# Performance work log

Hardware: AMD Instinct MI355X
Metric: run time of the kernel (lower is better)

Reference implementation:

```python
import jax, jax.numpy as jnp
import numpy as np

B, S, HID = 2, 2048, 2048
NH, NKV, HD = 16, 4, 128  # num_heads, num_kv_heads, head_dim; kqv_size = NH*HD = 2048
KV_DIM = NKV * HD  # 512


def setup_inputs() -> dict:
    key = jax.random.key(0)
    ks = jax.random.split(key, 7)
    sc = 0.02
    return {
        "hidden_states": jax.random.normal(ks[0], (B, S, HID), dtype=jnp.float32),
        "Wq": jax.random.normal(ks[1], (NH * HD, HID), dtype=jnp.float32) * sc,
        "Wk": jax.random.normal(ks[2], (KV_DIM, HID), dtype=jnp.float32) * sc,
        "Wv": jax.random.normal(ks[3], (KV_DIM, HID), dtype=jnp.float32) * sc,
        "Wo": jax.random.normal(ks[4], (HID, NH * HD), dtype=jnp.float32) * sc,
        "bo": jnp.zeros((HID,), dtype=jnp.float32),
    }


def reference(hidden_states, Wq, Wk, Wv, Wo, bo):
    b, s, _ = hidden_states.shape
    # projections (nn.Linear: x @ W.T), no bias on q/k/v
    q = (hidden_states @ Wq.T).reshape(b, s, NH, HD).transpose(0, 2, 1, 3)   # [B,NH,S,HD]
    k = (hidden_states @ Wk.T).reshape(b, s, NKV, HD).transpose(0, 2, 1, 3)  # [B,NKV,S,HD]
    v = (hidden_states @ Wv.T).reshape(b, s, NKV, HD).transpose(0, 2, 1, 3)
    # GQA: query head h uses kv head h // (NH // NKV)
    g = NH // NKV
    k_rep = jnp.repeat(k, g, axis=1)  # [B,NH,S,HD]
    v_rep = jnp.repeat(v, g, axis=1)
    # float32 upcast, NO 1/sqrt(d) scaling (GPT-Neo style)
    qf = q.astype(jnp.float32)
    kf = k_rep.astype(jnp.float32)
    scores = jnp.einsum("bhqd,bhkd->bhqk", qf, kf)  # [B,NH,S,S]
    causal = jnp.tril(jnp.ones((s, s), dtype=bool))[None, None]
    neg = jnp.finfo(scores.dtype).min
    scores = jnp.where(causal, scores, neg)
    attn = jax.nn.softmax(scores, axis=-1).astype(v.dtype)  # dropout p=0 (eval)
    out = jnp.einsum("bhqk,bhkd->bhqd", attn, v_rep)         # [B,NH,S,HD]
    out = out.transpose(0, 2, 1, 3).reshape(b, s, NH * HD)
    return out @ Wo.T + bo
```

## Files before the change

### kernel.cpp

```cpp
#include <hip/hip_runtime.h>

typedef _Float16 f16;
typedef __attribute__((ext_vector_type(4))) _Float16 f16x4;
typedef __attribute__((ext_vector_type(8))) _Float16 f16x8;
typedef __attribute__((ext_vector_type(4))) float f32x4;

#define NB 2
#define NS 2048
#define NHID 2048
#define N_H 16
#define N_KV 4
#define N_HD 128

__device__ __forceinline__ void gload16(void* lds, const void* g) {
  __builtin_amdgcn_global_load_lds(
      (const __attribute__((address_space(1))) unsigned int*)g,
      (__attribute__((address_space(3))) unsigned int*)lds, 16, 0, 0);
}

__global__ __launch_bounds__(256) void cvt_kernel(const float* __restrict__ in,
                                                  f16* __restrict__ out, int n4) {
  int i = blockIdx.x * 256 + threadIdx.x;
  if (i >= n4) return;
  const float4 v = reinterpret_cast<const float4*>(in)[i];
  f16x4 o = {(f16)v.x, (f16)v.y, (f16)v.z, (f16)v.w};
  reinterpret_cast<f16x4*>(out)[i] = o;
}

__global__ __launch_bounds__(256) void cvt3_kernel(const float* __restrict__ a, int na4,
                                                   const float* __restrict__ b, int nb4,
                                                   const float* __restrict__ c, int nc4,
                                                   f16* __restrict__ out) {
  int i = blockIdx.x * 256 + threadIdx.x;
  if (i >= na4 + nb4 + nc4) return;
  const float* src;
  int j;
  if (i < na4) { src = a; j = i; }
  else if (i < na4 + nb4) { src = b; j = i - na4; }
  else { src = c; j = i - na4 - nb4; }
  const float4 v = reinterpret_cast<const float4*>(src)[j];
  f16x4 o = {(f16)v.x, (f16)v.y, (f16)v.z, (f16)v.w};
  reinterpret_cast<f16x4*>(out)[i] = o;
}

template <int MODE>
__global__ __launch_bounds__(256) void gemm_bt(
    const f16* __restrict__ A, const f16* __restrict__ Bm, int K,
    f16* __restrict__ q_out, f16* __restrict__ k_out, f16* __restrict__ v_out,
    float* __restrict__ f_out, const float* __restrict__ bias) {
  __shared__ f16 Alds[128 * 32];
  __shared__ f16 Blds[128 * 32];
  const int t = threadIdx.x;
  const int l = t & 63;
  const int w = t >> 6;
  const int g = l >> 4;
  const int l15 = l & 15;
  const int mb = blockIdx.y, nb = blockIdx.x;
  const int wr = w >> 1, wc = w & 1;

  f32x4 acc[4][4] = {};
  const int nK = K >> 5;
  for (int kb = 0; kb < nK; ++kb) {
    __syncthreads();
#pragma unroll
    for (int it = 0; it < 2; ++it) {
      int cb = w * 128 + it * 64;
      int c = cb + l;
      int row = c >> 2, ci = c & 3;
      gload16(Alds + cb * 8, A + (size_t)(mb * 128 + row) * K + kb * 32 + ci * 8);
      gload16(Blds + cb * 8, Bm + (size_t)(nb * 128 + row) * K + kb * 32 + ci * 8);
    }
    asm volatile("s_waitcnt vmcnt(0)" ::: "memory");
    __syncthreads();

    f16x8 af[4], bf[4];
#pragma unroll
    for (int mi = 0; mi < 4; ++mi)
      af[mi] = *reinterpret_cast<const f16x8*>(Alds + (wr * 64 + mi * 16 + l15) * 32 + g * 8);
#pragma unroll
    for (int ni = 0; ni < 4; ++ni)
      bf[ni] = *reinterpret_cast<const f16x8*>(Blds + (wc * 64 + ni * 16 + l15) * 32 + g * 8);
#pragma unroll
    for (int mi = 0; mi < 4; ++mi)
#pragma unroll
      for (int ni = 0; ni < 4; ++ni)
        acc[mi][ni] = __builtin_amdgcn_mfma_f32_16x16x32_f16(af[mi], bf[ni], acc[mi][ni], 0, 0, 0);
  }

#pragma unroll
  for (int mi = 0; mi < 4; ++mi) {
    int m0 = mb * 128 + wr * 64 + mi * 16 + 4 * g;
#pragma unroll
    for (int ni = 0; ni < 4; ++ni) {
      int n = nb * 128 + wc * 64 + ni * 16 + l15;
#pragma unroll
      for (int r = 0; r < 4; ++r) {
        int mm = m0 + r;
        float val = acc[mi][ni][r];
        if (MODE == 0) {
          int b = mm >> 11, s = mm & (NS - 1);
          if (n < 2048) {
            int h = n >> 7, d = n & 127;
            q_out[(((size_t)(b * N_H + h)) * NS + s) * N_HD + d] = (f16)val;
          } else if (n < 2560) {
            int n2 = n - 2048, kvh = n2 >> 7, d = n2 & 127;
            k_out[(((size_t)(b * N_KV + kvh)) * NS + s) * N_HD + d] = (f16)val;
          } else {
            int n3 = n - 2560, kvh = n3 >> 7, d = n3 & 127;
            v_out[(((size_t)(b * N_KV + kvh)) * NS + s) * N_HD + d] = (f16)val;
          }
        } else {
          f_out[(size_t)mm * NHID + n] = val + bias[n];
        }
      }
    }
  }
}

__global__ __launch_bounds__(256) void transpose_v(const f16* __restrict__ V,
                                                   f16* __restrict__ Vt) {
  __shared__ f16 tt[64][72];
  int s0 = blockIdx.x * 64, d0 = blockIdx.y * 64, bk = blockIdx.z;
  const f16* Vp = V + (size_t)bk * NS * N_HD;
  f16* Vtp = Vt + (size_t)bk * N_HD * NS;
  int tid = threadIdx.x;
#pragma unroll
  for (int it = 0; it < 2; ++it) {
    int c = it * 256 + tid;
    int sr = c >> 3, dc = (c & 7) * 8;
    f16x8 v = *reinterpret_cast<const f16x8*>(Vp + (size_t)(s0 + sr) * N_HD + d0 + dc);
#pragma unroll
    for (int j = 0; j < 8; ++j) tt[dc + j][sr] = v[j];
  }
  __syncthreads();
#pragma unroll
  for (int it = 0; it < 2; ++it) {
    int c = it * 256 + tid;
    int dr = c >> 3, sc = (c & 7) * 8;
    f16x8 o;
#pragma unroll
    for (int j = 0; j < 8; ++j) o[j] = tt[dr][sc + j];
    *reinterpret_cast<f16x8*>(Vtp + (size_t)(d0 + dr) * NS + s0 + sc) = o;
  }
}

__device__ __forceinline__ void stage_kv(const f16* __restrict__ Kp,
                                         const f16* __restrict__ Vp,
                                         f16* Kl, f16* Vl, int kt, int w, int l) {
#pragma unroll
  for (int it = 0; it < 4; ++it) {
    int cb = (it * 4 + w) * 64;
    int c = cb + l;
    int krow = c >> 4, pch = c & 15;
    int sch = (pch & 8) | ((pch ^ krow) & 7);
    gload16(Kl + cb * 8, Kp + (size_t)(kt * 64 + krow) * N_HD + sch * 8);
  }
#pragma unroll
  for (int it = 0; it < 4; ++it) {
    int cb = (it * 4 + w) * 64;
    int c = cb + l;
    int drow = c >> 3, pch = c & 7;
    int sch = (pch ^ drow) & 7;
    gload16(Vl + cb * 8, Vp + (size_t)drow * NS + kt * 64 + sch * 8);
  }
}

__device__ __forceinline__ void attn_step(
    const f16x8* qf, f32x4* oacc, float* mrow, float* lrow, int q0, int kt,
    const f16* Kl, const f16* Vl, f16* Pw, int g, int l15, bool diag) {
  f32x4 sacc[4];
#pragma unroll
  for (int nt = 0; nt < 4; ++nt) {
    f32x4 z = {0.f, 0.f, 0.f, 0.f};
#pragma unroll
    for (int ks = 0; ks < 4; ++ks) {
      int kr = nt * 16 + l15;
      int ch = ks * 4 + g;
      int sw = (ch & 8) | ((ch ^ kr) & 7);
      f16x8 kf = *reinterpret_cast<const f16x8*>(Kl + kr * 128 + sw * 8);
      z = __builtin_amdgcn_mfma_f32_16x16x32_f16(qf[ks], kf, z, 0, 0, 0);
    }
    sacc[nt] = z;
  }

  float p[4][4], alpha[4];
#pragma unroll
  for (int r = 0; r < 4; ++r) {
    int qg = q0 + r;
    float mx = -3.0e38f;
#pragma unroll
    for (int nt = 0; nt < 4; ++nt) {
      float sv = sacc[nt][r];
      if (diag) {
        int kg = kt * 64 + nt * 16 + l15;
        if (kg > qg) sv = -3.0e38f;
      }
      p[nt][r] = sv;
      mx = fmaxf(mx, sv);
    }
#pragma unroll
    for (int off = 8; off >= 1; off >>= 1) mx = fmaxf(mx, __shfl_xor(mx, off));
    float mn = fmaxf(mrow[r], mx);
    alpha[r] = __expf(mrow[r] - mn);
    mrow[r] = mn;
    float rs = 0.f;
#pragma unroll
    for (int nt = 0; nt < 4; ++nt) {
      float pv = __expf(p[nt][r] - mn);
      p[nt][r] = pv;
      rs += pv;
    }
#pragma unroll
    for (int off = 8; off >= 1; off >>= 1) rs += __shfl_xor(rs, off);
    lrow[r] = lrow[r] * alpha[r] + rs;
  }
#pragma unroll
  for (int dt = 0; dt < 8; ++dt)
#pragma unroll
    for (int r = 0; r < 4; ++r) oacc[dt][r] *= alpha[r];

#pragma unroll
  for (int nt = 0; nt < 4; ++nt)
#pragma unroll
    for (int r = 0; r < 4; ++r) {
      int ql = 4 * g + r;
      int kp = nt * 16 + l15;
      int ch = kp >> 3;
      int idx = ql * 64 + (ch ^ (ql & 7)) * 8 + (kp & 7);
      Pw[idx] = (f16)p[nt][r];
    }
  asm volatile("s_waitcnt lgkmcnt(0)" ::: "memory");
  __builtin_amdgcn_sched_barrier(0);

  f16x8 pa[2];
#pragma unroll
  for (int ks2 = 0; ks2 < 2; ++ks2) {
    int ch = ks2 * 4 + g;
    pa[ks2] = *reinterpret_cast<const f16x8*>(&Pw[l15 * 64 + (ch ^ (l15 & 7)) * 8]);
  }
#pragma unroll
  for (int dt = 0; dt < 8; ++dt)
#pragma unroll
    for (int ks2 = 0; ks2 < 2; ++ks2) {
      int d = dt * 16 + l15;
      int ch = ks2 * 4 + g;
      f16x8 vf = *reinterpret_cast<const f16x8*>(Vl + d * 64 + (ch ^ (d & 7)) * 8);
      oacc[dt] = __builtin_amdgcn_mfma_f32_16x16x32_f16(pa[ks2], vf, oacc[dt], 0, 0, 0);
    }
}

__global__ __launch_bounds__(256, 2) void attn_kernel(
    const f16* __restrict__ Q, const f16* __restrict__ K,
    const f16* __restrict__ Vt, f16* __restrict__ O) {
  __shared__ f16 Klds[2][64 * 128];
  __shared__ f16 Vlds[2][128 * 64];
  __shared__ f16 Plds[4][16 * 64];
  const int t = threadIdx.x, l = t & 63, w = t >> 6;
  const int g = l >> 4, l15 = l & 15;
  const int pi = blockIdx.x;
  const int qtA = pi, qtB = 31 - pi;
  const int bh = blockIdx.y;
  const int b = bh >> 4, h = bh & 15;
  const int kvh = h >> 2;
  const f16* Qp = Q + ((size_t)(b * N_H + h)) * NS * N_HD;
  const f16* Kp = K + ((size_t)(b * N_KV + kvh)) * NS * N_HD;
  const f16* Vp = Vt + ((size_t)(b * N_KV + kvh)) * N_HD * NS;

  f16x8 qfA[4], qfB[4];
  const int qrA = qtA * 64 + w * 16 + l15;
  const int qrB = qtB * 64 + w * 16 + l15;
#pragma unroll
  for (int ks = 0; ks < 4; ++ks) {
    qfA[ks] = *reinterpret_cast<const f16x8*>(Qp + (size_t)qrA * N_HD + ks * 32 + g * 8);
    qfB[ks] = *reinterpret_cast<const f16x8*>(Qp + (size_t)qrB * N_HD + ks * 32 + g * 8);
  }

  f32x4 oA[8] = {}, oB[8] = {};
  float mA[4], lAr[4], mB[4], lBr[4];
#pragma unroll
  for (int r = 0; r < 4; ++r) {
    mA[r] = -3.0e38f; lAr[r] = 0.f;
    mB[r] = -3.0e38f; lBr[r] = 0.f;
  }
  const int q0A = qtA * 64 + w * 16 + 4 * g;
  const int q0B = qtB * 64 + w * 16 + 4 * g;

  const int nkt = qtB + 1;
  stage_kv(Kp, Vp, Klds[0], Vlds[0], 0, w, l);
  asm volatile("s_waitcnt vmcnt(0)" ::: "memory");
  __syncthreads();
  int cur = 0;
  for (int kt = 0; kt < nkt; ++kt) {
    if (kt + 1 < nkt)
      stage_kv(Kp, Vp, Klds[cur ^ 1], Vlds[cur ^ 1], kt + 1, w, l);
    attn_step(qfB, oB, mB, lBr, q0B, kt, Klds[cur], Vlds[cur], Plds[w], g, l15, kt == qtB);
    if (kt <= qtA)
      attn_step(qfA, oA, mA, lAr, q0A, kt, Klds[cur], Vlds[cur], Plds[w], g, l15, kt == qtA);
    asm volatile("s_waitcnt vmcnt(0)" ::: "memory");
    __syncthreads();
    cur ^= 1;
  }

#pragma unroll
  for (int r = 0; r < 4; ++r) {
    float invB = 1.0f / lBr[r];
    f16* orowB = O + (size_t)(b * NS + q0B + r) * NHID + h * N_HD;
#pragma unroll
    for (int dt = 0; dt < 8; ++dt) orowB[dt * 16 + l15] = (f16)(oB[dt][r] * invB);
    float invA = 1.0f / lAr[r];
    f16* orowA = O + (size_t)(b * NS + q0A + r) * NHID + h * N_HD;
#pragma unroll
    for (int dt = 0; dt < 8; ++dt) orowA[dt * 16 + l15] = (f16)(oA[dt][r] * invA);
  }
}

extern "C" void kernel_launch(void* const* d_in, const int* in_sizes, int n_in,
                              void* d_out, int out_size, void* d_ws, size_t ws_size,
                              hipStream_t stream) {
  const float* hs = (const float*)d_in[0];
  const float* Wq = (const float*)d_in[1];
  const float* Wk = (const float*)d_in[2];
  const float* Wv = (const float*)d_in[3];
  const float* Wo = (const float*)d_in[4];
  const float* bo = (const float*)d_in[5];
  float* out = (float*)d_out;

  char* ws = (char*)d_ws;
  f16* Xh   = (f16*)(ws);
  f16* Wqkv = (f16*)(ws + 16777216);
  f16* Woh  = (f16*)(ws + 29360128);
  f16* Qb   = (f16*)(ws + 37748736);
  f16* Kb   = (f16*)(ws + 54525952);
  f16* Vb   = (f16*)(ws + 58720256);
  f16* Vtb  = (f16*)(ws + 62914560);
  f16* Ob   = Xh;

  cvt_kernel<<<8192, 256, 0, stream>>>(hs, Xh, 2097152);
  cvt3_kernel<<<6144, 256, 0, stream>>>(Wq, 1048576, Wk, 262144, Wv, 262144, Wqkv);
  cvt_kernel<<<4096, 256, 0, stream>>>(Wo, Woh, 1048576);

  gemm_bt<0><<<dim3(24, 32), 256, 0, stream>>>(Xh, Wqkv, 2048, Qb, Kb, Vb, nullptr, nullptr);
  transpose_v<<<dim3(32, 2, 8), 256, 0, stream>>>(Vb, Vtb);
  attn_kernel<<<dim3(16, 32), 256, 0, stream>>>(Qb, Kb, Vtb, Ob);
  gemm_bt<1><<<dim3(16, 32), 256, 0, stream>>>(Ob, Woh, 2048, nullptr, nullptr, nullptr, out, bo);
}
```

Before: 238.0 us.

## Rewrite GEMMs as 8-wave multi-buffered pipelines and add lazy softmax rescaling

Replaces the single-buffered 128x128 GEMM with a 512-thread kernel using larger tiles (256x256 or 128x256) and a 4-deep LDS ring buffer that prefetches three k-steps ahead, with partial vmcnt waits, barriers and raised MFMA priority. In attention, Q is pre-scaled by log2(e) so exp2 can replace exp. The running-max rescale is skipped unless the max grows past a threshold, and s_setprio is placed around the MFMA sections. The lazy rescale and f16 scaling of Q slightly change numerics, and the larger tiles produce fewer blocks, which may underfill the GPU.

```diff
diff --git a/kernel.cpp b/kernel.cpp
--- a/kernel.cpp
+++ b/kernel.cpp
@@ -43,56 +43,128 @@
   reinterpret_cast<f16x4*>(out)[i] = o;
 }
 
-template <int MODE>
-__global__ __launch_bounds__(256) void gemm_bt(
-    const f16* __restrict__ A, const f16* __restrict__ Bm, int K,
+template <int MREP, int MODE>
+__global__ __launch_bounds__(512, 2) void gemm8(
+    const f16* __restrict__ A, const f16* __restrict__ Bm, const int K,
     f16* __restrict__ q_out, f16* __restrict__ k_out, f16* __restrict__ v_out,
     float* __restrict__ f_out, const float* __restrict__ bias) {
-  __shared__ f16 Alds[128 * 32];
-  __shared__ f16 Blds[128 * 32];
+  constexpr int BM = MREP * 32;
+  constexpr int GA = BM / 128;
+  constexpr int G = GA + 2;
+  constexpr int NPH = (MREP == 8) ? 2 : 1;
+  constexpr int ATILE = BM * 32;
+  constexpr int BTILE = 256 * 32;
+  constexpr int BUF = ATILE + BTILE;
+  __shared__ f16 lds[4 * BUF];
+
   const int t = threadIdx.x;
-  const int l = t & 63;
-  const int w = t >> 6;
-  const int g = l >> 4;
-  const int l15 = l & 15;
-  const int mb = blockIdx.y, nb = blockIdx.x;
-  const int wr = w >> 1, wc = w & 1;
-
-  f32x4 acc[4][4] = {};
-  const int nK = K >> 5;
-  for (int kb = 0; kb < nK; ++kb) {
-    __syncthreads();
-#pragma unroll
-    for (int it = 0; it < 2; ++it) {
-      int cb = w * 128 + it * 64;
-      int c = cb + l;
-      int row = c >> 2, ci = c & 3;
-      gload16(Alds + cb * 8, A + (size_t)(mb * 128 + row) * K + kb * 32 + ci * 8);
-      gload16(Blds + cb * 8, Bm + (size_t)(nb * 128 + row) * K + kb * 32 + ci * 8);
-    }
-    asm volatile("s_waitcnt vmcnt(0)" ::: "memory");
-    __syncthreads();
-
-    f16x8 af[4], bf[4];
-#pragma unroll
-    for (int mi = 0; mi < 4; ++mi)
-      af[mi] = *reinterpret_cast<const f16x8*>(Alds + (wr * 64 + mi * 16 + l15) * 32 + g * 8);
-#pragma unroll
-    for (int ni = 0; ni < 4; ++ni)
-      bf[ni] = *reinterpret_cast<const f16x8*>(Blds + (wc * 64 + ni * 16 + l15) * 32 + g * 8);
-#pragma unroll
-    for (int mi = 0; mi < 4; ++mi)
-#pragma unroll
-      for (int ni = 0; ni < 4; ++ni)
-        acc[mi][ni] = __builtin_amdgcn_mfma_f32_16x16x32_f16(af[mi], bf[ni], acc[mi][ni], 0, 0, 0);
-  }
-
-#pragma unroll
-  for (int mi = 0; mi < 4; ++mi) {
-    int m0 = mb * 128 + wr * 64 + mi * 16 + 4 * g;
+  const int l = t & 63, w = t >> 6;
+  const int g = l >> 4, l15 = l & 15;
+  const int wr = w >> 2, wc = w & 3;
+  const int nb = blockIdx.x, mb = blockIdx.y;
+  const int NT = K >> 5;
+
+  const f16* Aorig = A + (size_t)(mb * BM) * K;
+  const f16* Borig = Bm + (size_t)(nb * 256) * K;
+
+  size_t offA[GA], offB[2];
+#pragma unroll
+  for (int gi = 0; gi < GA; ++gi) {
+    int beta = gi * 8192 + t * 16;
+    int r = ((beta >> 9) << 3) | ((beta >> 4) & 7);
+    int c = (beta >> 7) & 3;
+    offA[gi] = (size_t)r * K + c * 8;
+  }
+#pragma unroll
+  for (int gj = 0; gj < 2; ++gj) {
+    int beta = gj * 8192 + t * 16;
+    int r = ((beta >> 9) << 3) | ((beta >> 4) & 7);
+    int c = (beta >> 7) & 3;
+    offB[gj] = (size_t)r * K + c * 8;
+  }
+
+  auto stage = [&](int kt, int gi) {
+    f16* bufbase = lds + (kt & 3) * BUF;
+    if (gi < GA) {
+      gload16(bufbase + gi * 4096 + w * 512, Aorig + offA[gi] + kt * 32);
+    } else {
+      int gj = gi - GA;
+      gload16(bufbase + ATILE + gj * 4096 + w * 512, Borig + offB[gj] + kt * 32);
+    }
+  };
+  const int fragoff = ((l15 >> 3) << 8) + (g << 6) + ((l15 & 7) << 3);
+  auto readA = [&](int kt, int mi) -> f16x8 {
+    int R0 = wr * (MREP * 16) + mi * 16;
+    return *reinterpret_cast<const f16x8*>(lds + (kt & 3) * BUF + R0 * 32 + fragoff);
+  };
+  auto readB = [&](int kt, int ni) -> f16x8 {
+    int R0 = wc * 64 + ni * 16;
+    return *reinterpret_cast<const f16x8*>(lds + (kt & 3) * BUF + ATILE + R0 * 32 + fragoff);
+  };
+
+  f32x4 acc[MREP][4] = {};
+
+#pragma unroll
+  for (int pt = 0; pt < 3; ++pt)
+#pragma unroll
+    for (int gi = 0; gi < G; ++gi) stage(pt, gi);
+  if constexpr (MREP == 8) asm volatile("s_waitcnt vmcnt(8)" ::: "memory");
+  else                     asm volatile("s_waitcnt vmcnt(6)" ::: "memory");
+  __builtin_amdgcn_s_barrier();
+
+  f16x8 bf[4];
+  for (int kt = 0; kt < NT; ++kt) {
+    const bool dostage = (kt + 3 < NT);
+#pragma unroll
+    for (int ph = 0; ph < NPH; ++ph) {
+      f16x8 af[4];
+#pragma unroll
+      for (int mi = 0; mi < 4; ++mi) af[mi] = readA(kt, ph * 4 + mi);
+      if (ph == 0) {
+#pragma unroll
+        for (int ni = 0; ni < 4; ++ni) bf[ni] = readB(kt, ni);
+      }
+      if (dostage) {
+        if constexpr (NPH == 2) {
+          stage(kt + 3, ph * 2);
+          stage(kt + 3, ph * 2 + 1);
+        } else {
+          stage(kt + 3, 0);
+          stage(kt + 3, 1);
+          stage(kt + 3, 2);
+        }
+      }
+      if (ph == NPH - 1) {
+        if (kt + 3 < NT) {
+          if constexpr (MREP == 8) asm volatile("s_waitcnt vmcnt(8)" ::: "memory");
+          else                     asm volatile("s_waitcnt vmcnt(6)" ::: "memory");
+        } else if (kt + 2 < NT) {
+          if constexpr (MREP == 8) asm volatile("s_waitcnt vmcnt(4)" ::: "memory");
+          else                     asm volatile("s_waitcnt vmcnt(3)" ::: "memory");
+        } else if (kt + 1 < NT) {
+          asm volatile("s_waitcnt vmcnt(0)" ::: "memory");
+        }
+      }
+      __builtin_amdgcn_s_barrier();
+      asm volatile("s_waitcnt lgkmcnt(0)" ::: "memory");
+      __builtin_amdgcn_s_setprio(1);
+#pragma unroll
+      for (int mi = 0; mi < 4; ++mi)
+#pragma unroll
+        for (int ni = 0; ni < 4; ++ni)
+          acc[ph * 4 + mi][ni] =
+              __builtin_amdgcn_mfma_f32_16x16x32_f16(af[mi], bf[ni], acc[ph * 4 + mi][ni], 0, 0, 0);
+      __builtin_amdgcn_s_setprio(0);
+      __builtin_amdgcn_s_barrier();
+    }
+  }
+
+#pragma unroll
+  for (int mi = 0; mi < MREP; ++mi) {
+    int m0 = mb * BM + wr * (MREP * 16) + mi * 16 + 4 * g;
 #pragma unroll
     for (int ni = 0; ni < 4; ++ni) {
-      int n = nb * 128 + wc * 64 + ni * 16 + l15;
+      int n = nb * 256 + wc * 64 + ni * 16 + l15;
 #pragma unroll
       for (int r = 0; r < 4; ++r) {
         int mm = m0 + r;
@@ -169,6 +241,7 @@
     const f16x8* qf, f32x4* oacc, float* mrow, float* lrow, int q0, int kt,
     const f16* Kl, const f16* Vl, f16* Pw, int g, int l15, bool diag) {
   f32x4 sacc[4];
+  __builtin_amdgcn_s_setprio(1);
 #pragma unroll
   for (int nt = 0; nt < 4; ++nt) {
     f32x4 z = {0.f, 0.f, 0.f, 0.f};
@@ -182,12 +255,14 @@
     }
     sacc[nt] = z;
   }
-
-  float p[4][4], alpha[4];
+  __builtin_amdgcn_s_setprio(0);
+
+  float p[4][4], mx[4];
+  bool need = false;
 #pragma unroll
   for (int r = 0; r < 4; ++r) {
     int qg = q0 + r;
-    float mx = -3.0e38f;
+    float m = -3.0e38f;
 #pragma unroll
     for (int nt = 0; nt < 4; ++nt) {
       float sv = sacc[nt][r];
@@ -196,28 +271,37 @@
         if (kg > qg) sv = -3.0e38f;
       }
       p[nt][r] = sv;
-      mx = fmaxf(mx, sv);
-    }
-#pragma unroll
-    for (int off = 8; off >= 1; off >>= 1) mx = fmaxf(mx, __shfl_xor(mx, off));
-    float mn = fmaxf(mrow[r], mx);
-    alpha[r] = __expf(mrow[r] - mn);
-    mrow[r] = mn;
+      m = fmaxf(m, sv);
+    }
+#pragma unroll
+    for (int off = 8; off >= 1; off >>= 1) m = fmaxf(m, __shfl_xor(m, off));
+    mx[r] = m;
+    need = need || (m > mrow[r] + 11.5f);
+  }
+  if (__any(need)) {
+#pragma unroll
+    for (int r = 0; r < 4; ++r) {
+      float m2 = fmaxf(mrow[r], mx[r]);
+      float alpha = __builtin_amdgcn_exp2f(mrow[r] - m2);
+      mrow[r] = m2;
+      lrow[r] *= alpha;
+#pragma unroll
+      for (int dt = 0; dt < 8; ++dt) oacc[dt][r] *= alpha;
+    }
+  }
+#pragma unroll
+  for (int r = 0; r < 4; ++r) {
     float rs = 0.f;
 #pragma unroll
     for (int nt = 0; nt < 4; ++nt) {
-      float pv = __expf(p[nt][r] - mn);
+      float pv = __builtin_amdgcn_exp2f(p[nt][r] - mrow[r]);
       p[nt][r] = pv;
       rs += pv;
     }
 #pragma unroll
     for (int off = 8; off >= 1; off >>= 1) rs += __shfl_xor(rs, off);
-    lrow[r] = lrow[r] * alpha[r] + rs;
-  }
-#pragma unroll
-  for (int dt = 0; dt < 8; ++dt)
-#pragma unroll
-    for (int r = 0; r < 4; ++r) oacc[dt][r] *= alpha[r];
+    lrow[r] += rs;
+  }
 
 #pragma unroll
   for (int nt = 0; nt < 4; ++nt)
@@ -238,6 +322,7 @@
     int ch = ks2 * 4 + g;
     pa[ks2] = *reinterpret_cast<const f16x8*>(&Pw[l15 * 64 + (ch ^ (l15 & 7)) * 8]);
   }
+  __builtin_amdgcn_s_setprio(1);
 #pragma unroll
   for (int dt = 0; dt < 8; ++dt)
 #pragma unroll
@@ -247,6 +332,7 @@
       f16x8 vf = *reinterpret_cast<const f16x8*>(Vl + d * 64 + (ch ^ (d & 7)) * 8);
       oacc[dt] = __builtin_amdgcn_mfma_f32_16x16x32_f16(pa[ks2], vf, oacc[dt], 0, 0, 0);
     }
+  __builtin_amdgcn_s_setprio(0);
 }
 
 __global__ __launch_bounds__(256, 2) void attn_kernel(
@@ -266,6 +352,7 @@
   const f16* Kp = K + ((size_t)(b * N_KV + kvh)) * NS * N_HD;
   const f16* Vp = Vt + ((size_t)(b * N_KV + kvh)) * N_HD * NS;
 
+  const f16 l2e = (f16)1.44269504f;
   f16x8 qfA[4], qfB[4];
   const int qrA = qtA * 64 + w * 16 + l15;
   const int qrB = qtB * 64 + w * 16 + l15;
@@ -273,6 +360,8 @@
   for (int ks = 0; ks < 4; ++ks) {
     qfA[ks] = *reinterpret_cast<const f16x8*>(Qp + (size_t)qrA * N_HD + ks * 32 + g * 8);
     qfB[ks] = *reinterpret_cast<const f16x8*>(Qp + (size_t)qrB * N_HD + ks * 32 + g * 8);
+#pragma unroll
+    for (int j = 0; j < 8; ++j) { qfA[ks][j] *= l2e; qfB[ks][j] *= l2e; }
   }
 
   f32x4 oA[8] = {}, oB[8] = {};
@@ -339,8 +428,8 @@
   cvt3_kernel<<<6144, 256, 0, stream>>>(Wq, 1048576, Wk, 262144, Wv, 262144, Wqkv);
   cvt_kernel<<<4096, 256, 0, stream>>>(Wo, Woh, 1048576);
 
-  gemm_bt<0><<<dim3(24, 32), 256, 0, stream>>>(Xh, Wqkv, 2048, Qb, Kb, Vb, nullptr, nullptr);
+  gemm8<8, 0><<<dim3(12, 16), 512, 0, stream>>>(Xh, Wqkv, 2048, Qb, Kb, Vb, nullptr, nullptr);
   transpose_v<<<dim3(32, 2, 8), 256, 0, stream>>>(Vb, Vtb);
   attn_kernel<<<dim3(16, 32), 256, 0, stream>>>(Qb, Kb, Vtb, Ob);
-  gemm_bt<1><<<dim3(16, 32), 256, 0, stream>>>(Ob, Woh, 2048, nullptr, nullptr, nullptr, out, bo);
-}
+  gemm8<4, 1><<<dim3(8, 32), 512, 0, stream>>>(Ob, Woh, 2048, nullptr, nullptr, nullptr, out, bo);
+}
```

Measured after the change: 239.8 us. Within noise of the previous version (+0.8%).
